# Optimization experiments

Hardware: AMD Instinct MI355X
Metric: run time of the kernel (lower is better)

The kernel has to match this reference:

```python
import jax, jax.numpy as jnp
import numpy as np

N_NODES = 500_000
N_EDGES = 16_000_000
D = 3  # node_representation_size hardcoded in the module


def setup_inputs() -> dict:
    key = jax.random.key(0)
    kx, kw, km, ks, kd = jax.random.split(key, 5)
    x = jax.random.normal(kx, (N_NODES, D), dtype=jnp.float32)
    # xavier_normal for a (3,3) matrix: std = sqrt(2/(3+3))
    std = float(np.sqrt(2.0 / (D + D)))
    W = jax.random.normal(kw, (D, D), dtype=jnp.float32) * std
    M = jax.random.normal(km, (D, D), dtype=jnp.float32) * std
    edge_src = jax.random.randint(ks, (N_EDGES,), 0, N_NODES, dtype=jnp.int32)
    edge_dst = jax.random.randint(kd, (N_EDGES,), 0, N_NODES, dtype=jnp.int32)
    return {"x": x, "W": W, "M": M, "edge_src": edge_src, "edge_dst": edge_dst}


def reference(x, W, M, edge_src, edge_dst):
    # Per-node: h_i = relu(x_i @ W + sum_{j in N(i)} x_j @ M)
    # Compute x @ M once, gather along edge sources, segment-sum into destinations.
    xm = x @ M                                   # [N, 3]
    agg = jax.ops.segment_sum(xm[edge_src], edge_dst, num_segments=N_NODES)  # [N, 3]
    h = jax.nn.relu(x @ W + agg)                 # [N, 3]
    s = jnp.sum(h, axis=0, keepdims=True)        # [1, 3] graph readout
    return jax.nn.softmax(s, axis=-1)            # F.softmax over last dim
```

## Files before the change

### kernel.cpp

```cpp
#include <hip/hip_runtime.h>
#include <hip/hip_fp16.h>

static constexpr int N_NODES = 500000;
static constexpr int N_EDGES = 16000000;

typedef int  iv4 __attribute__((ext_vector_type(4)));
typedef unsigned int uv4 __attribute__((ext_vector_type(4)));

static constexpr int BUCKET_SHIFT = 9;
static constexpr int BUCKET_NODES = 1 << BUCKET_SHIFT;
static constexpr int NB = (N_NODES + BUCKET_NODES - 1) >> BUCKET_SHIFT;
static constexpr int NBUCK = 1024;
static constexpr int CAP = 18432;
static constexpr int CHUNK = 10000;
static constexpr int BLOCKS_A = N_EDGES / CHUNK;

static constexpr size_t XMP_OFF  = 0;
static constexpr size_t SUMS_OFF = 4000000;
static constexpr size_t FILL_OFF = 4000064;
static constexpr size_t REC_OFF  = 4194304;
static constexpr size_t WS_NEEDED = REC_OFF + (size_t)NB * CAP * 4;

__device__ __forceinline__ void lds_pk_add_f16(unsigned int* gptr, unsigned int val) {
    unsigned addr = (unsigned)(size_t)(__attribute__((address_space(3))) unsigned int*)gptr;
    asm volatile("ds_pk_add_f16 %0, %1" :: "v"(addr), "v"(val) : "memory");
}


__global__ void prep_kernel(const float* __restrict__ x,
                            const float* __restrict__ M,
                            ushort4* __restrict__ xmp,
                            int* __restrict__ bucketFill,
                            double* __restrict__ sums) {
    int i = blockIdx.x * blockDim.x + threadIdx.x;
    if (i < NBUCK) bucketFill[i] = 0;
    if (i == 0) { sums[0] = 0.0; sums[1] = 0.0; sums[2] = 0.0; }
    if (i < N_NODES) {
        float m00 = M[0], m01 = M[1], m02 = M[2];
        float m10 = M[3], m11 = M[4], m12 = M[5];
        float m20 = M[6], m21 = M[7], m22 = M[8];
        float x0 = x[i * 3 + 0], x1 = x[i * 3 + 1], x2 = x[i * 3 + 2];
        float v0 = x0 * m00 + x1 * m10 + x2 * m20;
        float v1 = x0 * m01 + x1 * m11 + x2 * m21;
        float v2 = x0 * m02 + x1 * m12 + x2 * m22;
        ushort4 u;
        u.x = __half_as_ushort(__float2half_rn(v0));
        u.y = __half_as_ushort(__float2half_rn(v1));
        u.z = __half_as_ushort(__float2half_rn(v2));
        u.w = 0;
        xmp[i] = u;
    }
}

__global__ __launch_bounds__(512) void bin_kernel(const int* __restrict__ edge_src,
                                                  const int* __restrict__ edge_dst,
                                                  int* __restrict__ bucketFill,
                                                  unsigned int* __restrict__ records) {
    __shared__ int cnt[NBUCK];
    __shared__ unsigned short start[NBUCK];
    __shared__ unsigned short gbase[NBUCK];
    __shared__ int part[256];
    __shared__ unsigned int staged[CHUNK];

    const int t = threadIdx.x;
    const long e0 = (long)blockIdx.x * CHUNK;
    const iv4* __restrict__ dst4 = reinterpret_cast<const iv4*>(edge_dst + e0);
    const iv4* __restrict__ src4 = reinterpret_cast<const iv4*>(edge_src + e0);

    for (int b = t; b < NBUCK; b += 512) cnt[b] = 0;
    __syncthreads();

    for (int i = t; i < CHUNK / 4; i += 512) {
        iv4 d = __builtin_nontemporal_load(dst4 + i);
        atomicAdd(&cnt[d.x >> BUCKET_SHIFT], 1);
        atomicAdd(&cnt[d.y >> BUCKET_SHIFT], 1);
        atomicAdd(&cnt[d.z >> BUCKET_SHIFT], 1);
        atomicAdd(&cnt[d.w >> BUCKET_SHIFT], 1);
    }
    __syncthreads();

    int a0 = 0, a1 = 0, a2 = 0, a3 = 0, tsum = 0;
    if (t < 256) {
        a0 = cnt[4 * t + 0]; a1 = cnt[4 * t + 1]; a2 = cnt[4 * t + 2]; a3 = cnt[4 * t + 3];
        tsum = a0 + a1 + a2 + a3;
        part[t] = tsum;
    }
    __syncthreads();
    for (int off = 1; off < 256; off <<= 1) {
        int u = 0, v = 0;
        if (t < 256) { u = part[t]; v = (t >= off) ? part[t - off] : 0; }
        __syncthreads();
        if (t < 256) part[t] = u + v;
        __syncthreads();
    }
    if (t < 256) {
        int texcl = part[t] - tsum;
        start[4 * t + 0] = (unsigned short)texcl;
        start[4 * t + 1] = (unsigned short)(texcl + a0);
        start[4 * t + 2] = (unsigned short)(texcl + a0 + a1);
        start[4 * t + 3] = (unsigned short)(texcl + a0 + a1 + a2);
    }
    __syncthreads();

    for (int j = t; j < NBUCK; j += 512) {
        int b = (j + blockIdx.x * 7) & (NBUCK - 1);
        int c = cnt[b];
        gbase[b] = (unsigned short)((c > 0) ? atomicAdd(&bucketFill[b], c) : 0);
    }
    __syncthreads();
    for (int b = t; b < NBUCK; b += 512) cnt[b] = (int)start[b];
    __syncthreads();

    for (int i = t; i < CHUNK / 4; i += 512) {
        iv4 d = __builtin_nontemporal_load(dst4 + i);
        iv4 s = __builtin_nontemporal_load(src4 + i);
        int dd[4] = { d.x, d.y, d.z, d.w };
        int ss[4] = { s.x, s.y, s.z, s.w };
        #pragma unroll
        for (int k = 0; k < 4; ++k) {
            int b = dd[k] >> BUCKET_SHIFT;
            int r = atomicAdd(&cnt[b], 1);
            staged[r] = ((unsigned int)(dd[k] & (BUCKET_NODES - 1)) << 20) | (unsigned int)ss[k];
        }
    }
    __syncthreads();

    const int wv = t >> 6, ln = t & 63;
    for (int b = wv; b < NBUCK; b += 8) {
        int s0 = (int)start[b];
        int c  = cnt[b] - s0;
        int g  = (int)gbase[b];
        for (int i = ln; i < c; i += 64) {
            int pos = g + i;
            if (pos < CAP)
                __builtin_nontemporal_store(staged[s0 + i], &records[(size_t)b * CAP + pos]);
        }
    }
}

__global__ __launch_bounds__(1024) void bucket_kernel(const unsigned int* __restrict__ records,
                                                      const int* __restrict__ bucketFill,
                                                      const ushort4* __restrict__ xmp,
                                                      const float* __restrict__ x,
                                                      const float* __restrict__ W,
                                                      double* __restrict__ sums) {
    __shared__ unsigned int aggH2[BUCKET_NODES];
    __shared__ float        aggV2[BUCKET_NODES];
    __shared__ float        partw[16][3];

    const int b = blockIdx.x;
    const int t = threadIdx.x;
    const unsigned long long* __restrict__ xmp8 = (const unsigned long long*)xmp;

    for (int i = t; i < BUCKET_NODES; i += 1024) {
        aggH2[i] = 0u;
        aggV2[i] = 0.0f;
    }
    __syncthreads();

    int cnt = bucketFill[b];
    if (cnt > CAP) cnt = CAP;
    const unsigned int* __restrict__ rec = records + (size_t)b * CAP;
    const uv4* __restrict__ rec4 = reinterpret_cast<const uv4*>(rec);

    const int n4 = cnt >> 2;
    for (int i = t; i < n4; i += 1024) {
        uv4 r = __builtin_nontemporal_load(rec4 + i);
        unsigned int rr[4] = { r.x, r.y, r.z, r.w };
        unsigned long long g[4];
        #pragma unroll
        for (int k = 0; k < 4; ++k) g[k] = xmp8[rr[k] & 0xFFFFFu];
        __builtin_amdgcn_sched_barrier(0);
        #pragma unroll
        for (int k = 0; k < 4; ++k) {
            int dl = (int)(rr[k] >> 20);
            unsigned int u01 = (unsigned int)(g[k] & 0xFFFFFFFFull);
            lds_pk_add_f16(&aggH2[dl], u01);
            float v2 = __half2float(__ushort_as_half((unsigned short)((g[k] >> 32) & 0xFFFF)));
            atomicAdd(&aggV2[dl], v2);
        }
    }
    for (int i = (n4 << 2) + t; i < cnt; i += 1024) {
        unsigned int r = rec[i];
        unsigned long long g = xmp8[r & 0xFFFFFu];
        int dl = (int)(r >> 20);
        unsigned int u01 = (unsigned int)(g & 0xFFFFFFFFull);
        lds_pk_add_f16(&aggH2[dl], u01);
        float v2 = __half2float(__ushort_as_half((unsigned short)((g >> 32) & 0xFFFF)));
        atomicAdd(&aggV2[dl], v2);
    }
    __syncthreads();

    float s0 = 0.0f, s1 = 0.0f, s2 = 0.0f;
    if (t < BUCKET_NODES) {
        int node = (b << BUCKET_SHIFT) + t;
        if (node < N_NODES) {
            float w00 = W[0], w01 = W[1], w02 = W[2];
            float w10 = W[3], w11 = W[4], w12 = W[5];
            float w20 = W[6], w21 = W[7], w22 = W[8];
            float x0 = x[node * 3 + 0], x1 = x[node * 3 + 1], x2 = x[node * 3 + 2];
            unsigned int u = aggH2[t];
            float a0 = __half2float(__ushort_as_half((unsigned short)(u & 0xFFFF)));
            float a1 = __half2float(__ushort_as_half((unsigned short)(u >> 16)));
            float a2f = aggV2[t];
            float t0 = x0 * w00 + x1 * w10 + x2 * w20 + a0;
            float t1 = x0 * w01 + x1 * w11 + x2 * w21 + a1;
            float t2 = x0 * w02 + x1 * w12 + x2 * w22 + a2f;
            s0 = t0 > 0.0f ? t0 : 0.0f;
            s1 = t1 > 0.0f ? t1 : 0.0f;
            s2 = t2 > 0.0f ? t2 : 0.0f;
        }
    }

    #pragma unroll
    for (int off = 32; off > 0; off >>= 1) {
        s0 += __shfl_down(s0, off);
        s1 += __shfl_down(s1, off);
        s2 += __shfl_down(s2, off);
    }
    int lane = t & 63, wave = t >> 6;
    if (lane == 0) { partw[wave][0] = s0; partw[wave][1] = s1; partw[wave][2] = s2; }
    __syncthreads();
    if (t == 0) {
        double d0 = 0.0, d1 = 0.0, d2 = 0.0;
        #pragma unroll
        for (int w = 0; w < 16; ++w) {
            d0 += (double)partw[w][0];
            d1 += (double)partw[w][1];
            d2 += (double)partw[w][2];
        }
        atomicAdd(&sums[0], d0);
        atomicAdd(&sums[1], d1);
        atomicAdd(&sums[2], d2);
    }
}

__global__ void softmax_kernel(const double* __restrict__ sums,
                               float* __restrict__ out) {
    if (blockIdx.x == 0 && threadIdx.x == 0) {
        double s0 = sums[0], s1 = sums[1], s2 = sums[2];
        double m = fmax(s0, fmax(s1, s2));
        double e0 = exp(s0 - m), e1 = exp(s1 - m), e2 = exp(s2 - m);
        double tt = e0 + e1 + e2;
        out[0] = (float)(e0 / tt);
        out[1] = (float)(e1 / tt);
        out[2] = (float)(e2 / tt);
    }
}


__global__ void fb_precompute(const float* __restrict__ x, const float* __restrict__ M,
                              float* __restrict__ xm, float* __restrict__ agg,
                              double* __restrict__ sums) {
    int i = blockIdx.x * blockDim.x + threadIdx.x;
    if (i == 0) { sums[0] = 0.0; sums[1] = 0.0; sums[2] = 0.0; }
    if (i < N_NODES) {
        float m00 = M[0], m01 = M[1], m02 = M[2];
        float m10 = M[3], m11 = M[4], m12 = M[5];
        float m20 = M[6], m21 = M[7], m22 = M[8];
        float x0 = x[i * 3 + 0], x1 = x[i * 3 + 1], x2 = x[i * 3 + 2];
        xm[i * 3 + 0] = x0 * m00 + x1 * m10 + x2 * m20;
        xm[i * 3 + 1] = x0 * m01 + x1 * m11 + x2 * m21;
        xm[i * 3 + 2] = x0 * m02 + x1 * m12 + x2 * m22;
        agg[i * 3 + 0] = 0.0f; agg[i * 3 + 1] = 0.0f; agg[i * 3 + 2] = 0.0f;
    }
}

__global__ void fb_scatter(const int* __restrict__ edge_src, const int* __restrict__ edge_dst,
                           const float* __restrict__ xm, float* __restrict__ agg) {
    const int tid = blockIdx.x * blockDim.x + threadIdx.x;
    const int stride = gridDim.x * blockDim.x;
    const int4* src4 = reinterpret_cast<const int4*>(edge_src);
    const int4* dst4 = reinterpret_cast<const int4*>(edge_dst);
    const int n4 = N_EDGES / 4;
    for (int e = tid; e < n4; e += stride) {
        int4 s = src4[e]; int4 d = dst4[e];
        int ss[4] = { s.x, s.y, s.z, s.w };
        int dd[4] = { d.x, d.y, d.z, d.w };
        float v[4][3];
        #pragma unroll
        for (int k = 0; k < 4; ++k) {
            int bb = ss[k] * 3;
            v[k][0] = xm[bb + 0]; v[k][1] = xm[bb + 1]; v[k][2] = xm[bb + 2];
        }
        #pragma unroll
        for (int k = 0; k < 4; ++k) {
            int bb = dd[k] * 3;
            atomicAdd(&agg[bb + 0], v[k][0]);
            atomicAdd(&agg[bb + 1], v[k][1]);
            atomicAdd(&agg[bb + 2], v[k][2]);
        }
    }
}

__global__ void fb_reduce(const float* __restrict__ x, const float* __restrict__ W,
                          const float* __restrict__ agg, double* __restrict__ sums) {
    __shared__ float part[4][3];
    int i = blockIdx.x * blockDim.x + threadIdx.x;
    float h0 = 0.0f, h1 = 0.0f, h2 = 0.0f;
    if (i < N_NODES) {
        float w00 = W[0], w01 = W[1], w02 = W[2];
        float w10 = W[3], w11 = W[4], w12 = W[5];
        float w20 = W[6], w21 = W[7], w22 = W[8];
        float x0 = x[i * 3 + 0], x1 = x[i * 3 + 1], x2 = x[i * 3 + 2];
        float t0 = x0 * w00 + x1 * w10 + x2 * w20 + agg[i * 3 + 0];
        float t1 = x0 * w01 + x1 * w11 + x2 * w21 + agg[i * 3 + 1];
        float t2 = x0 * w02 + x1 * w12 + x2 * w22 + agg[i * 3 + 2];
        h0 = t0 > 0.0f ? t0 : 0.0f; h1 = t1 > 0.0f ? t1 : 0.0f; h2 = t2 > 0.0f ? t2 : 0.0f;
    }
    #pragma unroll
    for (int off = 32; off > 0; off >>= 1) {
        h0 += __shfl_down(h0, off); h1 += __shfl_down(h1, off); h2 += __shfl_down(h2, off);
    }
    int lane = threadIdx.x & 63, wave = threadIdx.x >> 6;
    if (lane == 0) { part[wave][0] = h0; part[wave][1] = h1; part[wave][2] = h2; }
    __syncthreads();
    if (threadIdx.x == 0) {
        double d0 = 0.0, d1 = 0.0, d2 = 0.0;
        #pragma unroll
        for (int w = 0; w < 4; ++w) {
            d0 += (double)part[w][0]; d1 += (double)part[w][1]; d2 += (double)part[w][2];
        }
        atomicAdd(&sums[0], d0); atomicAdd(&sums[1], d1); atomicAdd(&sums[2], d2);
    }
}


extern "C" void kernel_launch(void* const* d_in, const int* in_sizes, int n_in,
                              void* d_out, int out_size, void* d_ws, size_t ws_size,
                              hipStream_t stream) {
    const float* x        = (const float*)d_in[0];
    const float* W        = (const float*)d_in[1];
    const float* M        = (const float*)d_in[2];
    const int*   edge_src = (const int*)d_in[3];
    const int*   edge_dst = (const int*)d_in[4];
    float* out = (float*)d_out;

    char* ws = (char*)d_ws;
    const int nodeBlocks = (N_NODES + 255) / 256;

    if (ws_size >= WS_NEEDED) {
        ushort4*      xmp        = (ushort4*)(ws + XMP_OFF);
        double*       sums       = (double*)(ws + SUMS_OFF);
        int*          bucketFill = (int*)(ws + FILL_OFF);
        unsigned int* records    = (unsigned int*)(ws + REC_OFF);

        prep_kernel<<<nodeBlocks, 256, 0, stream>>>(x, M, xmp, bucketFill, sums);
        bin_kernel<<<BLOCKS_A, 512, 0, stream>>>(edge_src, edge_dst, bucketFill, records);
        bucket_kernel<<<NB, 1024, 0, stream>>>(records, bucketFill, xmp, x, W, sums);
        softmax_kernel<<<1, 1, 0, stream>>>(sums, out);
    } else {
        float*  xm   = (float*)ws;
        float*  agg  = xm + (size_t)N_NODES * 3;
        double* sums = (double*)(agg + (size_t)N_NODES * 3);

        fb_precompute<<<nodeBlocks, 256, 0, stream>>>(x, M, xm, agg, sums);
        fb_scatter<<<2048, 256, 0, stream>>>(edge_src, edge_dst, xm, agg);
        fb_reduce<<<nodeBlocks, 256, 0, stream>>>(x, W, agg, sums);
        softmax_kernel<<<1, 1, 0, stream>>>(sums, out);
    }
}
```

Baseline: 348.2 us.

## Replace count-scan binning with fixed-capacity per-bucket LDS staging and overflow atomics

The binning kernel no longer does a counting pass, a prefix scan and a per-bucket global reservation before scattering. Each edge now goes into a fixed 16-slot LDS stage per bucket, and any overflow is written straight to global memory through a per-element global atomic on bucketFill. The flush step assigns 16 lanes per bucket, and one lane reserves the global range. This removes a second read of edge_dst and several barriers. In exchange, about 10000/1024 ≈ 10 edges per bucket on average fit in 16 slots, so buckets that exceed that pay a global atomic per edge, and their records land scattered and uncoalesced.

```diff
diff --git a/kernel.cpp b/kernel.cpp
--- a/kernel.cpp
+++ b/kernel.cpp
@@ -14,6 +14,7 @@
 static constexpr int CAP = 18432;
 static constexpr int CHUNK = 10000;
 static constexpr int BLOCKS_A = N_EDGES / CHUNK;
+static constexpr int CAP_S = 16;
 
 static constexpr size_t XMP_OFF  = 0;
 static constexpr size_t SUMS_OFF = 4000000;
@@ -57,10 +58,7 @@
                                                   int* __restrict__ bucketFill,
                                                   unsigned int* __restrict__ records) {
     __shared__ int cnt[NBUCK];
-    __shared__ unsigned short start[NBUCK];
-    __shared__ unsigned short gbase[NBUCK];
-    __shared__ int part[256];
-    __shared__ unsigned int staged[CHUNK];
+    __shared__ unsigned int stage[NBUCK * CAP_S];
 
     const int t = threadIdx.x;
     const long e0 = (long)blockIdx.x * CHUNK;
@@ -68,47 +66,6 @@
     const iv4* __restrict__ src4 = reinterpret_cast<const iv4*>(edge_src + e0);
 
     for (int b = t; b < NBUCK; b += 512) cnt[b] = 0;
-    __syncthreads();
-
-    for (int i = t; i < CHUNK / 4; i += 512) {
-        iv4 d = __builtin_nontemporal_load(dst4 + i);
-        atomicAdd(&cnt[d.x >> BUCKET_SHIFT], 1);
-        atomicAdd(&cnt[d.y >> BUCKET_SHIFT], 1);
-        atomicAdd(&cnt[d.z >> BUCKET_SHIFT], 1);
-        atomicAdd(&cnt[d.w >> BUCKET_SHIFT], 1);
-    }
-    __syncthreads();
-
-    int a0 = 0, a1 = 0, a2 = 0, a3 = 0, tsum = 0;
-    if (t < 256) {
-        a0 = cnt[4 * t + 0]; a1 = cnt[4 * t + 1]; a2 = cnt[4 * t + 2]; a3 = cnt[4 * t + 3];
-        tsum = a0 + a1 + a2 + a3;
-        part[t] = tsum;
-    }
-    __syncthreads();
-    for (int off = 1; off < 256; off <<= 1) {
-        int u = 0, v = 0;
-        if (t < 256) { u = part[t]; v = (t >= off) ? part[t - off] : 0; }
-        __syncthreads();
-        if (t < 256) part[t] = u + v;
-        __syncthreads();
-    }
-    if (t < 256) {
-        int texcl = part[t] - tsum;
-        start[4 * t + 0] = (unsigned short)texcl;
-        start[4 * t + 1] = (unsigned short)(texcl + a0);
-        start[4 * t + 2] = (unsigned short)(texcl + a0 + a1);
-        start[4 * t + 3] = (unsigned short)(texcl + a0 + a1 + a2);
-    }
-    __syncthreads();
-
-    for (int j = t; j < NBUCK; j += 512) {
-        int b = (j + blockIdx.x * 7) & (NBUCK - 1);
-        int c = cnt[b];
-        gbase[b] = (unsigned short)((c > 0) ? atomicAdd(&bucketFill[b], c) : 0);
-    }
-    __syncthreads();
-    for (int b = t; b < NBUCK; b += 512) cnt[b] = (int)start[b];
     __syncthreads();
 
     for (int i = t; i < CHUNK / 4; i += 512) {
@@ -119,21 +76,31 @@
         #pragma unroll
         for (int k = 0; k < 4; ++k) {
             int b = dd[k] >> BUCKET_SHIFT;
+            unsigned int rec = ((unsigned int)(dd[k] & (BUCKET_NODES - 1)) << 20) | (unsigned int)ss[k];
             int r = atomicAdd(&cnt[b], 1);
-            staged[r] = ((unsigned int)(dd[k] & (BUCKET_NODES - 1)) << 20) | (unsigned int)ss[k];
+            if (r < CAP_S) {
+                stage[b * CAP_S + r] = rec;
+            } else {
+                int pos = atomicAdd(&bucketFill[b], 1);
+                if (pos < CAP)
+                    __builtin_nontemporal_store(rec, &records[(size_t)b * CAP + pos]);
+            }
         }
     }
     __syncthreads();
 
     const int wv = t >> 6, ln = t & 63;
-    for (int b = wv; b < NBUCK; b += 8) {
-        int s0 = (int)start[b];
-        int c  = cnt[b] - s0;
-        int g  = (int)gbase[b];
-        for (int i = ln; i < c; i += 64) {
+    const int grp = ln >> 4, q = ln & 15;
+    for (int b = wv * 4 + grp; b < NBUCK; b += 32) {
+        int c = cnt[b];
+        if (c > CAP_S) c = CAP_S;
+        int g = 0;
+        if (q == 0 && c > 0) g = atomicAdd(&bucketFill[b], c);
+        g = __shfl(g, ln & 48);
+        for (int i = q; i < c; i += 16) {
             int pos = g + i;
             if (pos < CAP)
-                __builtin_nontemporal_store(staged[s0 + i], &records[(size_t)b * CAP + pos]);
+                __builtin_nontemporal_store(stage[b * CAP_S + i], &records[(size_t)b * CAP + pos]);
         }
     }
 }
@@ -174,8 +141,7 @@
         #pragma unroll
         for (int k = 0; k < 4; ++k) {
             int dl = (int)(rr[k] >> 20);
-            unsigned int u01 = (unsigned int)(g[k] & 0xFFFFFFFFull);
-            lds_pk_add_f16(&aggH2[dl], u01);
+            lds_pk_add_f16(&aggH2[dl], (unsigned int)(g[k] & 0xFFFFFFFFull));
             float v2 = __half2float(__ushort_as_half((unsigned short)((g[k] >> 32) & 0xFFFF)));
             atomicAdd(&aggV2[dl], v2);
         }
@@ -184,8 +150,7 @@
         unsigned int r = rec[i];
         unsigned long long g = xmp8[r & 0xFFFFFu];
         int dl = (int)(r >> 20);
-        unsigned int u01 = (unsigned int)(g & 0xFFFFFFFFull);
-        lds_pk_add_f16(&aggH2[dl], u01);
+        lds_pk_add_f16(&aggH2[dl], (unsigned int)(g & 0xFFFFFFFFull));
         float v2 = __half2float(__ushort_as_half((unsigned short)((g >> 32) & 0xFFFF)));
         atomicAdd(&aggV2[dl], v2);
     }
```

New measurement: 446.6 us. +28.3%, slower.
